# Kernel optimization log

Hardware: AMD Instinct MI355X
Metric: run time of the kernel (lower is better)

## Reference

```python
import jax, jax.numpy as jnp
import numpy as np

B, S, D, H = 2, 2048, 1024, 16
DK = D // H


def setup_inputs() -> dict:
    key = jax.random.key(0)
    ks = jax.random.split(key, 12)
    scale = 1.0 / np.sqrt(D)
    inp = {
        "query": jax.random.normal(ks[0], (B, S, D), jnp.float32),
        "key_in": jax.random.normal(ks[1], (B, S, D), jnp.float32),
        "value": jax.random.normal(ks[2], (B, S, D), jnp.float32),
        "mask": jnp.ones((1, 1, S, S), dtype=bool),
        "w_q": jax.random.normal(ks[3], (D, D), jnp.float32) * scale,
        "b_q": jnp.zeros((D,), jnp.float32),
        "w_k": jax.random.normal(ks[4], (D, D), jnp.float32) * scale,
        "b_k": jnp.zeros((D,), jnp.float32),
        "w_v": jax.random.normal(ks[5], (D, D), jnp.float32) * scale,
        "b_v": jnp.zeros((D,), jnp.float32),
        "w_o": jax.random.normal(ks[6], (D, D), jnp.float32) * scale,
        "b_o": jnp.zeros((D,), jnp.float32),
    }
    return inp


def reference(query, key_in, value, mask, w_q, b_q, w_k, b_k, w_v, b_v, w_o, b_o):
    # QKV projections (nn.Linear: x @ W.T + b; here weights stored as [D_in, D_out])
    q = query @ w_q + b_q          # [B, S, D]
    k = key_in @ w_k + b_k
    v = value @ w_v + b_v
    # split heads -> [B, H, S, DK]
    q = q.reshape(B, S, H, DK).transpose(0, 2, 1, 3)
    k = k.reshape(B, S, H, DK).transpose(0, 2, 1, 3)
    v = v.reshape(B, S, H, DK).transpose(0, 2, 1, 3)
    # scaled dot-product attention (naive: full [B,H,S,S] scores)
    scores = jnp.einsum('bhqd,bhkd->bhqk', q, k) / jnp.sqrt(jnp.float32(DK))
    scores = jnp.where(mask, scores, jnp.float32(-1e9))
    probs = jax.nn.softmax(scores, axis=-1)  # dropout p=0.0 -> identity
    x = jnp.einsum('bhqk,bhkd->bhqd', probs, v)  # [B, H, S, DK]
    x = x.transpose(0, 2, 1, 3).reshape(B, S, D)
    return x @ w_o + b_o
```

## Files before the change

kernel.cpp:

```cpp
#include <hip/hip_runtime.h>
#include <cstdint>
#include <cstddef>


typedef _Float16 f16_t;
typedef _Float16 f16x8 __attribute__((ext_vector_type(8)));
typedef _Float16 f16x4 __attribute__((ext_vector_type(4)));
typedef float    f32x4 __attribute__((ext_vector_type(4)));

#define S_LEN 2048
#define DMODEL 1024
#define NHEAD 16
#define DK 64

__device__ __forceinline__ void async_copy16(void* lds, const void* g) {
    __builtin_amdgcn_global_load_lds(
        (const __attribute__((address_space(1))) unsigned int*)g,
        (__attribute__((address_space(3))) unsigned int*)lds,
        16, 0, 0);
}

__global__ __launch_bounds__(256) void cvt3_kernel(
    const float* __restrict__ s0, const float* __restrict__ s1, const float* __restrict__ s2,
    f16_t* __restrict__ d0, f16_t* __restrict__ d1, f16_t* __restrict__ d2, int n)
{
    const float* s = blockIdx.y == 0 ? s0 : blockIdx.y == 1 ? s1 : s2;
    f16_t*       d = blockIdx.y == 0 ? d0 : blockIdx.y == 1 ? d1 : d2;
    int i = (blockIdx.x * 256 + threadIdx.x) * 4;
    if (i + 3 < n) {
        f32x4 v = *(const f32x4*)(s + i);
        f16x4 o;
        o[0] = (f16_t)v[0]; o[1] = (f16_t)v[1];
        o[2] = (f16_t)v[2]; o[3] = (f16_t)v[3];
        *(f16x4*)(d + i) = o;
    }
}

__global__ __launch_bounds__(256) void transpose_cvt_kernel(
    const float* __restrict__ w0, const float* __restrict__ w1,
    const float* __restrict__ w2, const float* __restrict__ w3,
    f16_t* __restrict__ wt_base)
{
    __shared__ float tile[32][33];
    int z = blockIdx.z;
    const float* w = z == 0 ? w0 : z == 1 ? w1 : z == 2 ? w2 : w3;
    f16_t* wt = wt_base + (size_t)z * DMODEL * DMODEL;
    int tx = threadIdx.x, ty = threadIdx.y;
    int bx = blockIdx.x * 32;
    int by = blockIdx.y * 32;
#pragma unroll
    for (int i = 0; i < 4; ++i)
        tile[ty + i * 8][tx] = w[(size_t)(bx + ty + i * 8) * DMODEL + by + tx];
    __syncthreads();
#pragma unroll
    for (int i = 0; i < 4; ++i)
        wt[(size_t)(by + ty + i * 8) * DMODEL + bx + tx] = (f16_t)tile[tx][ty + i * 8];
}

__global__ __launch_bounds__(256) void qkv_gemm_kernel(
    const f16_t* __restrict__ Aq, const f16_t* __restrict__ Ak, const f16_t* __restrict__ Av,
    const f16_t* __restrict__ Bt,
    const float* __restrict__ bq, const float* __restrict__ bk, const float* __restrict__ bv,
    f16_t* __restrict__ q_h, f16_t* __restrict__ k_h, f16_t* __restrict__ v_t)
{
    __shared__ f16_t As[128 * 32];
    __shared__ f16_t Bs[128 * 32];

    int tid  = threadIdx.x;
    int lane = tid & 63;
    int w    = tid >> 6;
    int wm   = w >> 1, wn = w & 1;
    int row0 = blockIdx.y * 128;
    int col0 = blockIdx.x * 128;
    int which = col0 >> 10;
    const f16_t* A = which == 0 ? Aq : which == 1 ? Ak : Av;
    const float* bias = which == 0 ? bq : which == 1 ? bk : bv;

    f32x4 acc[4][4] = {};

    for (int kk = 0; kk < 1024; kk += 32) {
        __syncthreads();
#pragma unroll
        for (int j = 0; j < 2; ++j) {
            int c = w * 2 + j;
            int r = c * 16 + (lane >> 2);
            int e = (lane & 3) * 8;
            async_copy16(&As[c * 512], A  + (size_t)(row0 + r) * 1024 + kk + e);
            async_copy16(&Bs[c * 512], Bt + (size_t)(col0 + r) * 1024 + kk + e);
        }
        __syncthreads();

        f16x8 a[4], b[4];
#pragma unroll
        for (int mi = 0; mi < 4; ++mi)
            a[mi] = *(const f16x8*)&As[(wm * 64 + mi * 16 + (lane & 15)) * 32 + (lane >> 4) * 8];
#pragma unroll
        for (int ni = 0; ni < 4; ++ni)
            b[ni] = *(const f16x8*)&Bs[(wn * 64 + ni * 16 + (lane & 15)) * 32 + (lane >> 4) * 8];
#pragma unroll
        for (int mi = 0; mi < 4; ++mi)
#pragma unroll
            for (int ni = 0; ni < 4; ++ni)
                acc[mi][ni] = __builtin_amdgcn_mfma_f32_16x16x32_f16(a[mi], b[ni], acc[mi][ni], 0, 0, 0);
    }

#pragma unroll
    for (int mi = 0; mi < 4; ++mi) {
#pragma unroll
        for (int ni = 0; ni < 4; ++ni) {
#pragma unroll
            for (int r = 0; r < 4; ++r) {
                int grow = row0 + wm * 64 + mi * 16 + (lane >> 4) * 4 + r;
                int gcol = col0 + wn * 64 + ni * 16 + (lane & 15);
                int nc   = gcol & 1023;
                float v  = acc[mi][ni][r] + bias[nc];
                int bb = grow >> 11, ss = grow & 2047;
                int hh = nc >> 6,    dd = nc & 63;
                if (which == 0)
                    q_h[(((size_t)(bb * NHEAD + hh) * S_LEN + ss) << 6) + dd] = (f16_t)(v * 0.125f);
                else if (which == 1)
                    k_h[(((size_t)(bb * NHEAD + hh) * S_LEN + ss) << 6) + dd] = (f16_t)v;
                else
                    v_t[((size_t)(bb * NHEAD + hh) * DK + dd) * S_LEN + ss] = (f16_t)v;
            }
        }
    }
}

__global__ __launch_bounds__(256) void out_gemm_kernel(
    const f16_t* __restrict__ A, const f16_t* __restrict__ Bt,
    const float* __restrict__ bias, float* __restrict__ outp)
{
    __shared__ f16_t As[128 * 32];
    __shared__ f16_t Bs[128 * 32];

    int tid  = threadIdx.x;
    int lane = tid & 63;
    int w    = tid >> 6;
    int wm   = w >> 1, wn = w & 1;
    int row0 = blockIdx.y * 128;
    int col0 = blockIdx.x * 128;

    f32x4 acc[4][4] = {};

    for (int kk = 0; kk < 1024; kk += 32) {
        __syncthreads();
#pragma unroll
        for (int j = 0; j < 2; ++j) {
            int c = w * 2 + j;
            int r = c * 16 + (lane >> 2);
            int e = (lane & 3) * 8;
            async_copy16(&As[c * 512], A  + (size_t)(row0 + r) * 1024 + kk + e);
            async_copy16(&Bs[c * 512], Bt + (size_t)(col0 + r) * 1024 + kk + e);
        }
        __syncthreads();

        f16x8 a[4], b[4];
#pragma unroll
        for (int mi = 0; mi < 4; ++mi)
            a[mi] = *(const f16x8*)&As[(wm * 64 + mi * 16 + (lane & 15)) * 32 + (lane >> 4) * 8];
#pragma unroll
        for (int ni = 0; ni < 4; ++ni)
            b[ni] = *(const f16x8*)&Bs[(wn * 64 + ni * 16 + (lane & 15)) * 32 + (lane >> 4) * 8];
#pragma unroll
        for (int mi = 0; mi < 4; ++mi)
#pragma unroll
            for (int ni = 0; ni < 4; ++ni)
                acc[mi][ni] = __builtin_amdgcn_mfma_f32_16x16x32_f16(a[mi], b[ni], acc[mi][ni], 0, 0, 0);
    }

#pragma unroll
    for (int mi = 0; mi < 4; ++mi)
#pragma unroll
        for (int ni = 0; ni < 4; ++ni)
#pragma unroll
            for (int r = 0; r < 4; ++r) {
                int grow = row0 + wm * 64 + mi * 16 + (lane >> 4) * 4 + r;
                int gcol = col0 + wn * 64 + ni * 16 + (lane & 15);
                outp[(size_t)grow * 1024 + gcol] = acc[mi][ni][r] + bias[gcol];
            }
}

__global__ __launch_bounds__(256) void flash_kernel(
    const f16_t* __restrict__ Q, const f16_t* __restrict__ K,
    const f16_t* __restrict__ Vt, f16_t* __restrict__ Ao)
{
    __shared__ f16_t Kl[64 * 64];
    __shared__ f16_t Vl[64 * 64];
    __shared__ f16_t Pw[4][32 * 72];

    int tid  = threadIdx.x;
    int lane = tid & 63;
    int li   = lane & 15;
    int g    = lane >> 4;
    int w    = tid >> 6;
    int qt   = blockIdx.x;
    int bh   = blockIdx.y;
    const size_t hbase = (size_t)bh * S_LEN * DK;
    const f16_t* Qh = Q  + hbase;
    const f16_t* Kh = K  + hbase;
    const f16_t* Vh = Vt + hbase;

    int q0 = qt * 128 + w * 32;

    f16x8 aq[2][2];
#pragma unroll
    for (int qc = 0; qc < 2; ++qc)
#pragma unroll
        for (int kc = 0; kc < 2; ++kc)
            aq[qc][kc] = *(const f16x8*)(Qh + (size_t)(q0 + qc * 16 + li) * DK + kc * 32 + g * 8);

    f32x4 o[2][4] = {};
    float mrun[2] = {-1e30f, -1e30f};
    float lrun[2] = {0.f, 0.f};

    for (int kt = 0; kt < S_LEN / 64; ++kt) {
        __syncthreads();
#pragma unroll
        for (int j = 0; j < 2; ++j) {
            int r0  = w * 16 + j * 8;
            int row = r0 + (lane >> 3);
            int sl  = (lane & 7) ^ (row & 7);
            async_copy16(&Kl[r0 * 64], Kh + (size_t)(kt * 64 + row) * 64 + sl * 8);
            async_copy16(&Vl[r0 * 64], Vh + (size_t)row * S_LEN + kt * 64 + sl * 8);
        }
        __syncthreads();

        f32x4 s[4][2] = {};
#pragma unroll
        for (int kc = 0; kc < 2; ++kc)
#pragma unroll
            for (int kn = 0; kn < 4; ++kn) {
                int row = kn * 16 + li;
                int sp  = (kc * 4 + g) ^ (row & 7);
                f16x8 ak = *(const f16x8*)&Kl[row * 64 + sp * 8];
                s[kn][0] = __builtin_amdgcn_mfma_f32_16x16x32_f16(ak, aq[0][kc], s[kn][0], 0, 0, 0);
                s[kn][1] = __builtin_amdgcn_mfma_f32_16x16x32_f16(ak, aq[1][kc], s[kn][1], 0, 0, 0);
            }

        float alpha[2];
#pragma unroll
        for (int qc = 0; qc < 2; ++qc) {
            float mx = -1e30f;
#pragma unroll
            for (int kn = 0; kn < 4; ++kn)
#pragma unroll
                for (int r = 0; r < 4; ++r)
                    mx = fmaxf(mx, s[kn][qc][r]);
            mx = fmaxf(mx, __shfl_xor(mx, 16));
            mx = fmaxf(mx, __shfl_xor(mx, 32));
            float mn = fmaxf(mrun[qc], mx);
            alpha[qc] = __expf(mrun[qc] - mn);
            mrun[qc] = mn;
            float rs = 0.f;
#pragma unroll
            for (int kn = 0; kn < 4; ++kn) {
                f16x4 pv;
#pragma unroll
                for (int r = 0; r < 4; ++r) {
                    float p = __expf(s[kn][qc][r] - mn);
                    rs += p;
                    pv[r] = (f16_t)p;
                }
                *(f16x4*)&Pw[w][(qc * 16 + li) * 72 + kn * 16 + g * 4] = pv;
            }
            rs += __shfl_xor(rs, 16);
            rs += __shfl_xor(rs, 32);
            lrun[qc] = lrun[qc] * alpha[qc] + rs;
        }

#pragma unroll
        for (int qr = 0; qr < 2; ++qr)
#pragma unroll
            for (int r = 0; r < 4; ++r) {
                float av = __shfl(alpha[qr], g * 4 + r);
#pragma unroll
                for (int nd = 0; nd < 4; ++nd)
                    o[qr][nd][r] *= av;
            }

#pragma unroll
        for (int kc = 0; kc < 2; ++kc) {
            f16x8 pa0 = *(const f16x8*)&Pw[w][(0 * 16 + li) * 72 + kc * 32 + g * 8];
            f16x8 pa1 = *(const f16x8*)&Pw[w][(1 * 16 + li) * 72 + kc * 32 + g * 8];
#pragma unroll
            for (int nd = 0; nd < 4; ++nd) {
                int row = nd * 16 + li;
                int sp  = (kc * 4 + g) ^ (row & 7);
                f16x8 bv = *(const f16x8*)&Vl[row * 64 + sp * 8];
                o[0][nd] = __builtin_amdgcn_mfma_f32_16x16x32_f16(pa0, bv, o[0][nd], 0, 0, 0);
                o[1][nd] = __builtin_amdgcn_mfma_f32_16x16x32_f16(pa1, bv, o[1][nd], 0, 0, 0);
            }
        }
    }

    int b = bh >> 4, h = bh & 15;
#pragma unroll
    for (int qr = 0; qr < 2; ++qr)
#pragma unroll
        for (int r = 0; r < 4; ++r) {
            float lr  = __shfl(lrun[qr], g * 4 + r);
            float inv = 1.0f / lr;
            int row = q0 + qr * 16 + g * 4 + r;
            size_t base = (size_t)(b * S_LEN + row) * DMODEL + h * 64;
#pragma unroll
            for (int nd = 0; nd < 4; ++nd)
                Ao[base + nd * 16 + li] = (f16_t)(o[qr][nd][r] * inv);
        }
}

extern "C" void kernel_launch(void* const* d_in, const int* in_sizes, int n_in,
                              void* d_out, int out_size, void* d_ws, size_t ws_size,
                              hipStream_t stream)
{
    const float* query  = (const float*)d_in[0];
    const float* key_in = (const float*)d_in[1];
    const float* value  = (const float*)d_in[2];
    const float* w_q = (const float*)d_in[4];
    const float* b_q = (const float*)d_in[5];
    const float* w_k = (const float*)d_in[6];
    const float* b_k = (const float*)d_in[7];
    const float* w_v = (const float*)d_in[8];
    const float* b_v = (const float*)d_in[9];
    const float* w_o = (const float*)d_in[10];
    const float* b_o = (const float*)d_in[11];
    float* out = (float*)d_out;

    char* ws = (char*)d_ws;
    const size_t MB = 1024 * 1024;
    f16_t* x_q  = (f16_t*)(ws + 0 * MB);
    f16_t* x_k  = (f16_t*)(ws + 8 * MB);
    f16_t* x_v  = (f16_t*)(ws + 16 * MB);
    f16_t* wt   = (f16_t*)(ws + 24 * MB);
    f16_t* wt_o = (f16_t*)(ws + 30 * MB);
    f16_t* q_h  = (f16_t*)(ws + 32 * MB);
    f16_t* k_h  = (f16_t*)(ws + 40 * MB);
    f16_t* v_t  = (f16_t*)(ws + 48 * MB);
    f16_t* attn = (f16_t*)(ws + 56 * MB);

    const int n = 2 * S_LEN * DMODEL;

    cvt3_kernel<<<dim3(n / 1024, 3), 256, 0, stream>>>(query, key_in, value, x_q, x_k, x_v, n);
    transpose_cvt_kernel<<<dim3(32, 32, 4), dim3(32, 8), 0, stream>>>(w_q, w_k, w_v, w_o, wt);

    qkv_gemm_kernel<<<dim3(24, 32), 256, 0, stream>>>(
        x_q, x_k, x_v, wt, b_q, b_k, b_v, q_h, k_h, v_t);

    flash_kernel<<<dim3(S_LEN / 128, 32), 256, 0, stream>>>(q_h, k_h, v_t, attn);

    out_gemm_kernel<<<dim3(8, 32), 256, 0, stream>>>(attn, wt_o, b_o, out);
}
```

Measured before the change: 164.9 us.

## Double-buffer K/V tiles, use exp2 softmax, and transpose PV accumulator for vector stores

Flash attention now double-buffers K/V tiles in LDS, prefetching the next tile asynchronously while the current one is computed, which removes one barrier per iteration and aims to hide load latency. The softmax folds log2(e) into the Q scale so it can use the hardware exp2 directly. The PV MFMA operands are swapped so the output accumulator is transposed, which removes the per-row alpha shuffles and lets the output be written as 4-wide vector stores. It also adds setprio around the MFMA sections. The cost is double the K/V LDS use, which may lower occupancy, and there is a possible race: the async copies may not be waited on before the next barrier.

```diff
diff --git a/kernel.cpp b/kernel.cpp
--- a/kernel.cpp
+++ b/kernel.cpp
@@ -18,6 +18,14 @@
         (const __attribute__((address_space(1))) unsigned int*)g,
         (__attribute__((address_space(3))) unsigned int*)lds,
         16, 0, 0);
+}
+
+__device__ __forceinline__ float fexp2(float x) {
+#if __has_builtin(__builtin_amdgcn_exp2f)
+    return __builtin_amdgcn_exp2f(x);
+#else
+    return exp2f(x);
+#endif
 }
 
 __global__ __launch_bounds__(256) void cvt3_kernel(
@@ -104,6 +112,7 @@
                 acc[mi][ni] = __builtin_amdgcn_mfma_f32_16x16x32_f16(a[mi], b[ni], acc[mi][ni], 0, 0, 0);
     }
 
+    const float QSCALE = 0.125f * 1.4426950408889634f;
 #pragma unroll
     for (int mi = 0; mi < 4; ++mi) {
 #pragma unroll
@@ -117,7 +126,7 @@
                 int bb = grow >> 11, ss = grow & 2047;
                 int hh = nc >> 6,    dd = nc & 63;
                 if (which == 0)
-                    q_h[(((size_t)(bb * NHEAD + hh) * S_LEN + ss) << 6) + dd] = (f16_t)(v * 0.125f);
+                    q_h[(((size_t)(bb * NHEAD + hh) * S_LEN + ss) << 6) + dd] = (f16_t)(v * QSCALE);
                 else if (which == 1)
                     k_h[(((size_t)(bb * NHEAD + hh) * S_LEN + ss) << 6) + dd] = (f16_t)v;
                 else
@@ -185,8 +194,8 @@
     const f16_t* __restrict__ Q, const f16_t* __restrict__ K,
     const f16_t* __restrict__ Vt, f16_t* __restrict__ Ao)
 {
-    __shared__ f16_t Kl[64 * 64];
-    __shared__ f16_t Vl[64 * 64];
+    __shared__ f16_t Kl[2][64 * 64];
+    __shared__ f16_t Vl[2][64 * 64];
     __shared__ f16_t Pw[4][32 * 72];
 
     int tid  = threadIdx.x;
@@ -210,35 +219,42 @@
         for (int kc = 0; kc < 2; ++kc)
             aq[qc][kc] = *(const f16x8*)(Qh + (size_t)(q0 + qc * 16 + li) * DK + kc * 32 + g * 8);
 
-    f32x4 o[2][4] = {};
+    f32x4 ot[2][4] = {};
     float mrun[2] = {-1e30f, -1e30f};
     float lrun[2] = {0.f, 0.f};
 
-    for (int kt = 0; kt < S_LEN / 64; ++kt) {
-        __syncthreads();
+    auto stage = [&](int buf, int kt) {
 #pragma unroll
         for (int j = 0; j < 2; ++j) {
             int r0  = w * 16 + j * 8;
             int row = r0 + (lane >> 3);
             int sl  = (lane & 7) ^ (row & 7);
-            async_copy16(&Kl[r0 * 64], Kh + (size_t)(kt * 64 + row) * 64 + sl * 8);
-            async_copy16(&Vl[r0 * 64], Vh + (size_t)row * S_LEN + kt * 64 + sl * 8);
-        }
-        __syncthreads();
+            async_copy16(&Kl[buf][r0 * 64], Kh + (size_t)(kt * 64 + row) * 64 + sl * 8);
+            async_copy16(&Vl[buf][r0 * 64], Vh + (size_t)row * S_LEN + kt * 64 + sl * 8);
+        }
+    };
+
+    stage(0, 0);
+    int cur = 0;
+
+    for (int kt = 0; kt < S_LEN / 64; ++kt) {
+        __syncthreads();
+        if (kt + 1 < S_LEN / 64) stage(cur ^ 1, kt + 1);
 
         f32x4 s[4][2] = {};
+        __builtin_amdgcn_s_setprio(1);
 #pragma unroll
         for (int kc = 0; kc < 2; ++kc)
 #pragma unroll
             for (int kn = 0; kn < 4; ++kn) {
                 int row = kn * 16 + li;
                 int sp  = (kc * 4 + g) ^ (row & 7);
-                f16x8 ak = *(const f16x8*)&Kl[row * 64 + sp * 8];
+                f16x8 ak = *(const f16x8*)&Kl[cur][row * 64 + sp * 8];
                 s[kn][0] = __builtin_amdgcn_mfma_f32_16x16x32_f16(ak, aq[0][kc], s[kn][0], 0, 0, 0);
                 s[kn][1] = __builtin_amdgcn_mfma_f32_16x16x32_f16(ak, aq[1][kc], s[kn][1], 0, 0, 0);
             }
-
-        float alpha[2];
+        __builtin_amdgcn_s_setprio(0);
+
 #pragma unroll
         for (int qc = 0; qc < 2; ++qc) {
             float mx = -1e30f;
@@ -250,7 +266,7 @@
             mx = fmaxf(mx, __shfl_xor(mx, 16));
             mx = fmaxf(mx, __shfl_xor(mx, 32));
             float mn = fmaxf(mrun[qc], mx);
-            alpha[qc] = __expf(mrun[qc] - mn);
+            float alpha = fexp2(mrun[qc] - mn);
             mrun[qc] = mn;
             float rs = 0.f;
 #pragma unroll
@@ -258,7 +274,7 @@
                 f16x4 pv;
 #pragma unroll
                 for (int r = 0; r < 4; ++r) {
-                    float p = __expf(s[kn][qc][r] - mn);
+                    float p = fexp2(s[kn][qc][r] - mn);
                     rs += p;
                     pv[r] = (f16_t)p;
                 }
@@ -266,47 +282,48 @@
             }
             rs += __shfl_xor(rs, 16);
             rs += __shfl_xor(rs, 32);
-            lrun[qc] = lrun[qc] * alpha[qc] + rs;
-        }
-
-#pragma unroll
-        for (int qr = 0; qr < 2; ++qr)
-#pragma unroll
-            for (int r = 0; r < 4; ++r) {
-                float av = __shfl(alpha[qr], g * 4 + r);
-#pragma unroll
-                for (int nd = 0; nd < 4; ++nd)
-                    o[qr][nd][r] *= av;
-            }
-
+            lrun[qc] = lrun[qc] * alpha + rs;
+#pragma unroll
+            for (int nd = 0; nd < 4; ++nd)
+#pragma unroll
+                for (int r = 0; r < 4; ++r)
+                    ot[qc][nd][r] *= alpha;
+        }
+
+        __builtin_amdgcn_s_setprio(1);
 #pragma unroll
         for (int kc = 0; kc < 2; ++kc) {
-            f16x8 pa0 = *(const f16x8*)&Pw[w][(0 * 16 + li) * 72 + kc * 32 + g * 8];
-            f16x8 pa1 = *(const f16x8*)&Pw[w][(1 * 16 + li) * 72 + kc * 32 + g * 8];
+            f16x8 bp0 = *(const f16x8*)&Pw[w][(0 * 16 + li) * 72 + kc * 32 + g * 8];
+            f16x8 bp1 = *(const f16x8*)&Pw[w][(1 * 16 + li) * 72 + kc * 32 + g * 8];
 #pragma unroll
             for (int nd = 0; nd < 4; ++nd) {
                 int row = nd * 16 + li;
                 int sp  = (kc * 4 + g) ^ (row & 7);
-                f16x8 bv = *(const f16x8*)&Vl[row * 64 + sp * 8];
-                o[0][nd] = __builtin_amdgcn_mfma_f32_16x16x32_f16(pa0, bv, o[0][nd], 0, 0, 0);
-                o[1][nd] = __builtin_amdgcn_mfma_f32_16x16x32_f16(pa1, bv, o[1][nd], 0, 0, 0);
-            }
-        }
+                f16x8 av = *(const f16x8*)&Vl[cur][row * 64 + sp * 8];
+                ot[0][nd] = __builtin_amdgcn_mfma_f32_16x16x32_f16(av, bp0, ot[0][nd], 0, 0, 0);
+                ot[1][nd] = __builtin_amdgcn_mfma_f32_16x16x32_f16(av, bp1, ot[1][nd], 0, 0, 0);
+            }
+        }
+        __builtin_amdgcn_s_setprio(0);
+
+        cur ^= 1;
     }
 
     int b = bh >> 4, h = bh & 15;
 #pragma unroll
-    for (int qr = 0; qr < 2; ++qr)
-#pragma unroll
-        for (int r = 0; r < 4; ++r) {
-            float lr  = __shfl(lrun[qr], g * 4 + r);
-            float inv = 1.0f / lr;
-            int row = q0 + qr * 16 + g * 4 + r;
-            size_t base = (size_t)(b * S_LEN + row) * DMODEL + h * 64;
-#pragma unroll
-            for (int nd = 0; nd < 4; ++nd)
-                Ao[base + nd * 16 + li] = (f16_t)(o[qr][nd][r] * inv);
-        }
+    for (int qc = 0; qc < 2; ++qc) {
+        float inv = 1.0f / lrun[qc];
+        int qrow = q0 + qc * 16 + li;
+        size_t base = (size_t)(b * S_LEN + qrow) * DMODEL + h * 64;
+#pragma unroll
+        for (int nd = 0; nd < 4; ++nd) {
+            f16x4 ov;
+#pragma unroll
+            for (int r = 0; r < 4; ++r)
+                ov[r] = (f16_t)(ot[qc][nd][r] * inv);
+            *(f16x4*)&((f16_t*)Ao)[base + nd * 16 + g * 4] = ov;
+        }
+    }
 }
 
 extern "C" void kernel_launch(void* const* d_in, const int* in_sizes, int n_in,
```

New measurement: 157.0 us. -4.8%, faster.
